# Kernel optimization log

Measured on AMD Instinct MI355X. Metric: run time of the kernel, lower is better.

Reference implementation:

```python
import jax, jax.numpy as jnp
import numpy as np

T, B, N = 256, 128, 64
START_IDX, END_IDX = 1, 2  # Offsets.GO, Offsets.EOS
NEG = -10000.0


def setup_inputs() -> dict:
    key = jax.random.key(0)
    k1, k2, k3 = jax.random.split(key, 3)
    unary = jax.random.normal(k1, (T, B, N), dtype=jnp.float32)          # [T, B, N] emissions
    trans = jax.random.normal(k2, (1, N, N), dtype=jnp.float32) * 0.1    # [1, N_to, N_from]
    lengths = jax.random.randint(k3, (B,), 1, T + 1)                      # 1 <= len <= T
    return {"unary": unary, "trans": trans, "lengths": lengths}


def _crf_log_partition(unary, trans, lengths):
    # unary: [T, B, N], trans: [1, N, N], lengths: [B] -> [B] log Z
    batch_size, n_tags = unary.shape[1], unary.shape[2]
    alphas0 = jnp.full((batch_size, 1, n_tags), NEG, dtype=unary.dtype)
    alphas0 = alphas0.at[:, 0, START_IDX].set(0.0)

    def step(alphas, xi):
        unary_t, i = xi  # unary_t: [B, N], i: scalar timestep
        # scores[b, to, fr] = alphas[b, 0, fr] + trans[0, to, fr] + unary_t[b, to]
        scores = alphas + trans + unary_t[:, :, None]            # [B, N, N]
        new_alphas = jax.nn.logsumexp(scores, axis=2)[:, None, :]  # [B, 1, N]
        # keep new alphas while the sequence is still active (i < length),
        # otherwise carry the old alphas forward (matches masked_fill logic).
        alphas = jnp.where((i < lengths)[:, None, None], new_alphas, alphas)
        return alphas, None

    steps = jnp.arange(unary.shape[0])
    alphas, _ = jax.lax.scan(step, alphas0, (unary, steps))
    terminal = alphas + trans[:, END_IDX]                         # [B, 1, N]
    return jax.nn.logsumexp(terminal, axis=2).squeeze(1)          # [B]


def reference(unary, trans, lengths):
    return _crf_log_partition(unary, trans, lengths)
```

## Files before the change

kernel.cpp:

```cpp
#include <hip/hip_runtime.h>

#define T_STEPS 256
#define B_SIZE  128
#define N_TAGS  64
#define BN_     8192
#define SEGS    16
#define SEGL    16
#define START_IDX 1
#define END_IDX 2

typedef float  f32x4  __attribute__((ext_vector_type(4)));
typedef float  f32x2  __attribute__((ext_vector_type(2)));
typedef short  bf16x8 __attribute__((ext_vector_type(8)));

union U8 { unsigned u[4]; bf16x8 v; };
union F4 { f32x4 v; f32x2 h[2]; float f[4]; };

__device__ __forceinline__ float fexp2(float x){float r;asm("v_exp_f32 %0, %1":"=v"(r):"v"(x));return r;}
__device__ __forceinline__ float flog2(float x){float r;asm("v_log_f32 %0, %1":"=v"(r):"v"(x));return r;}
__device__ __forceinline__ float frcp(float x){float r;asm("v_rcp_f32 %0, %1":"=v"(r):"v"(x));return r;}
__device__ __forceinline__ unsigned cvtpk(float lo,float hi){unsigned r;asm("v_cvt_pk_bf16_f32 %0, %1, %2":"=v"(r):"v"(lo),"v"(hi));return r;}
__device__ __forceinline__ void swap32(unsigned &a, unsigned &b){asm("v_permlane32_swap_b32 %0, %1":"+v"(a),"+v"(b));}
__device__ __forceinline__ void swap16(unsigned &a, unsigned &b){asm("v_permlane16_swap_b32 %0, %1":"+v"(a),"+v"(b));}
__device__ __forceinline__ f32x2 pkmul(f32x2 a, f32x2 b){f32x2 r;asm("v_pk_mul_f32 %0, %1, %2":"=v"(r):"v"(a),"v"(b));return r;}

#define MFMA16(A, B, C) __builtin_amdgcn_mfma_f32_16x16x32_bf16(A, B, C, 0, 0, 0)

__device__ __forceinline__ void wait24(){ asm volatile("s_waitcnt vmcnt(24)" ::: "memory"); __builtin_amdgcn_sched_barrier(0); }
__device__ __forceinline__ void wait16(){ asm volatile("s_waitcnt vmcnt(16)" ::: "memory"); __builtin_amdgcn_sched_barrier(0); }
__device__ __forceinline__ void wait8 (){ asm volatile("s_waitcnt vmcnt(8)"  ::: "memory"); __builtin_amdgcn_sched_barrier(0); }
__device__ __forceinline__ void wait0 (){ asm volatile("s_waitcnt vmcnt(0)"  ::: "memory"); __builtin_amdgcn_sched_barrier(0); }
__device__ __forceinline__ void wait28(){ asm volatile("s_waitcnt vmcnt(28)" ::: "memory"); __builtin_amdgcn_sched_barrier(0); }

#define IDP() do { _Pragma("unroll") \
  for (int c=0;c<2;++c) { _Pragma("unroll") \
    for (int cc=0;cc<4;++cc) { _Pragma("unroll") \
      for (int m=0;m<4;++m) { \
        int k0 = 32*c + 8*g + 2*m, n = 16*cc + col; \
        unsigned lo = (k0==n)?0x3F80u:0u, hi=(k0+1==n)?0x3F80u:0u; \
        P[c][cc].u[m] = lo | (hi<<16); } } } } while(0)

#define EVG() do { _Pragma("unroll") \
  for (int tt=0;tt<4;++tt) { _Pragma("unroll") \
    for (int r=0;r<4;++r) ev[tt][r] = __shfl(eul, 16*tt + 4*g + r, 64); } } while(0)

#define EVSCALE() do { _Pragma("unroll") \
  for (int tt=0;tt<4;++tt) { f32x2 e01,e23; \
    e01[0]=ev[tt][0]; e01[1]=ev[tt][1]; e23[0]=ev[tt][2]; e23[1]=ev[tt][3]; \
    _Pragma("unroll") for (int cc=0;cc<4;++cc) { \
      Dt[tt][cc].h[0]=pkmul(Dt[tt][cc].h[0],e01); \
      Dt[tt][cc].h[1]=pkmul(Dt[tt][cc].h[1],e23); } } } while(0)

#define RESC() do { float mm = Dt[0][0].f[0]; \
  _Pragma("unroll") for (int tt=0;tt<4;++tt) { _Pragma("unroll") for (int cc=0;cc<4;++cc) { \
    _Pragma("unroll") for (int r=0;r<4;++r) mm = fmaxf(mm, Dt[tt][cc].f[r]); } } \
  _Pragma("unroll") for (int m2=1;m2<64;m2<<=1) mm = fmaxf(mm, __shfl_xor(mm,m2,64)); \
  float inv = frcp(mm); C += LN2*flog2(mm); \
  f32x2 iv; iv[0]=inv; iv[1]=inv; \
  _Pragma("unroll") for (int tt=0;tt<4;++tt) { _Pragma("unroll") for (int cc=0;cc<4;++cc) { \
    Dt[tt][cc].h[0]=pkmul(Dt[tt][cc].h[0],iv); Dt[tt][cc].h[1]=pkmul(Dt[tt][cc].h[1],iv); } } } while(0)

#define CVTP() do { _Pragma("unroll") \
  for (int cc=0;cc<4;++cc) { \
    unsigned p00 = cvtpk(Dt[0][cc].f[0], Dt[0][cc].f[1]); \
    unsigned p01 = cvtpk(Dt[0][cc].f[2], Dt[0][cc].f[3]); \
    unsigned p10 = cvtpk(Dt[1][cc].f[0], Dt[1][cc].f[1]); \
    unsigned p11 = cvtpk(Dt[1][cc].f[2], Dt[1][cc].f[3]); \
    unsigned p20 = cvtpk(Dt[2][cc].f[0], Dt[2][cc].f[1]); \
    unsigned p21 = cvtpk(Dt[2][cc].f[2], Dt[2][cc].f[3]); \
    unsigned p30 = cvtpk(Dt[3][cc].f[0], Dt[3][cc].f[1]); \
    unsigned p31 = cvtpk(Dt[3][cc].f[2], Dt[3][cc].f[3]); \
    swap32(p00, p10); swap32(p01, p11); swap32(p20, p30); swap32(p21, p31); \
    swap16(p00, p10); swap16(p01, p11); swap16(p20, p30); swap16(p21, p31); \
    P[0][cc].u[0]=p00; P[0][cc].u[1]=p01; P[0][cc].u[2]=p10; P[0][cc].u[3]=p11; \
    P[1][cc].u[0]=p20; P[1][cc].u[1]=p21; P[1][cc].u[2]=p30; P[1][cc].u[3]=p31; } } while(0)

#define MFMAB() do { _Pragma("unroll") \
  for (int cc=0;cc<4;++cc) { _Pragma("unroll") \
    for (int tt=0;tt<4;++tt) { \
      f32x4 acc = MFMA16(EA[tt][0].v, P[0][cc].v, zf); \
      Dt[tt][cc].v = MFMA16(EA[tt][1].v, P[1][cc].v, acc); } } } while(0)

#define STOREP() do { _Pragma("unroll") \
  for (int cc=0;cc<4;++cc) { _Pragma("unroll") \
    for (int c=0;c<2;++c) { \
      uint4 q; q.x=P[c][cc].u[0]; q.y=P[c][cc].u[1]; q.z=P[c][cc].u[2]; q.w=P[c][cc].u[3]; \
      *(uint4*)(dst + (cc*2+c)*256) = q; } } } while(0)

__global__ __launch_bounds__(64, 2)
void crf_seg_kernel(const float* __restrict__ u, const float* __restrict__ trans,
                    const int* __restrict__ lengths,
                    unsigned* __restrict__ Mout, float* __restrict__ Cout) {
    const int bid  = blockIdx.x;
    const int b    = bid & (B_SIZE - 1);
    const int s    = bid >> 7;
    const int lane = threadIdx.x;
    const int col  = lane & 15;
    const int g    = lane >> 4;
    const float K = 1.4426950408889634f, LN2 = 0.6931471805599453f;
    const f32x4 zf = {0.f, 0.f, 0.f, 0.f};

    const int len = lengths[b];
    int n_act = len - 1 - s*SEGL;
    n_act = max(0, min(SEGL, n_act));
    unsigned* dst = Mout + (size_t)(b*SEGS + s) * 2048 + lane * 4;

    U8 P[2][4];
    if (n_act == 0) {
        IDP();
        STOREP();
        if (lane == 0) Cout[b*SEGS + s] = 0.0f;
        return;
    }

    __shared__ __align__(16) float sT[N_TAGS * N_TAGS];
    {
        const float4* t4 = (const float4*)trans;
        float4* s4 = (float4*)sT;
#pragma unroll
        for (int k = 0; k < 16; ++k) s4[k*64 + lane] = t4[k*64 + lane];
    }
    __syncthreads();

    const bool front = (s < 8);
    U8 EA[4][2];
    if (!front) {
#pragma unroll
        for (int tt = 0; tt < 4; ++tt) {
#pragma unroll
            for (int c = 0; c < 2; ++c) {
                const float* p = &sT[(16*tt + col)*64 + 32*c + 8*g];
#pragma unroll
                for (int j2 = 0; j2 < 4; ++j2)
                    EA[tt][c].u[j2] = cvtpk(fexp2(p[2*j2]*K), fexp2(p[2*j2+1]*K));
            }
        }
    } else {
#pragma unroll
        for (int tt = 0; tt < 4; ++tt) {
#pragma unroll
            for (int c = 0; c < 2; ++c) {
#pragma unroll
                for (int j2 = 0; j2 < 4; ++j2) {
                    const int a0 = 32*c + 8*g + 2*j2;
                    EA[tt][c].u[j2] = cvtpk(fexp2(sT[a0*64 + 16*tt + col] * K),
                                            fexp2(sT[(a0+1)*64 + 16*tt + col] * K));
                }
            }
        }
    }

    F4 Dt[4][4];
    float C = 0.0f;
    float ev[4][4];
    const float* ub = u + (size_t)b * 64 + lane;

    if (!front) {
        IDP();
        const int t0 = 16*s + 1;
        float uc = ub[(size_t)t0 * BN_];
        float un = ub[(size_t)min(t0 + 1, T_STEPS - 1) * BN_];
        for (int i = 0; i < n_act; ++i) {
            float eul = fexp2(uc * K);
            uc = un; un = ub[(size_t)min(t0 + i + 2, T_STEPS - 1) * BN_];
            EVG();
            MFMAB();
            EVSCALE();
            if ((i & 7) == 7) RESC();
            CVTP();
        }
    } else {
#pragma unroll
        for (int tt = 0; tt < 4; ++tt) {
#pragma unroll
            for (int cc = 0; cc < 4; ++cc) {
#pragma unroll
                for (int r = 0; r < 4; ++r)
                    Dt[tt][cc].f[r] = (tt == cc && 4*g + r == col) ? 1.0f : 0.0f;
            }
        }
        const int th = 16*s + n_act;
        float uc = ub[(size_t)th * BN_];
        float un = ub[(size_t)max(th - 1, 0) * BN_];
        for (int i = 0; i < n_act; ++i) {
            float eul = fexp2(uc * K);
            uc = un; un = ub[(size_t)max(th - i - 2, 0) * BN_];
            EVG();
            EVSCALE();
            if ((i & 7) == 7) RESC();
            CVTP();
            MFMAB();
        }
        CVTP();
    }

    STOREP();
    if (lane == 0) Cout[b*SEGS + s] = C;
}

#define MLOAD(SL, SEG) do { \
    const unsigned* _mp = mbase + (size_t)(SEG) * 2048; \
    const unsigned* _mq = _mp + 1024; \
    asm volatile("global_load_dwordx4 %0, %1, off"             : "=v"(SL[0].v) : "v"(_mp)); \
    asm volatile("global_load_dwordx4 %0, %1, off offset:1024" : "=v"(SL[1].v) : "v"(_mp)); \
    asm volatile("global_load_dwordx4 %0, %1, off offset:2048" : "=v"(SL[2].v) : "v"(_mp)); \
    asm volatile("global_load_dwordx4 %0, %1, off offset:3072" : "=v"(SL[3].v) : "v"(_mp)); \
    asm volatile("global_load_dwordx4 %0, %1, off"             : "=v"(SL[4].v) : "v"(_mq)); \
    asm volatile("global_load_dwordx4 %0, %1, off offset:1024" : "=v"(SL[5].v) : "v"(_mq)); \
    asm volatile("global_load_dwordx4 %0, %1, off offset:2048" : "=v"(SL[6].v) : "v"(_mq)); \
    asm volatile("global_load_dwordx4 %0, %1, off offset:3072" : "=v"(SL[7].v) : "v"(_mq)); \
} while (0)

#define PSTEP(WN, SL, LD) do { \
    wait##WN(); \
    U8 Af0, Af1; \
    { float vs = (g < 2) ? a0 : a1; \
      float f0=__shfl(vs,sbase+0,64), f1=__shfl(vs,sbase+1,64); \
      float f2=__shfl(vs,sbase+2,64), f3=__shfl(vs,sbase+3,64); \
      float f4=__shfl(vs,sbase+4,64), f5=__shfl(vs,sbase+5,64); \
      float f6=__shfl(vs,sbase+6,64), f7=__shfl(vs,sbase+7,64); \
      Af0.u[0]=cvtpk(f0,f1); Af0.u[1]=cvtpk(f2,f3); Af0.u[2]=cvtpk(f4,f5); Af0.u[3]=cvtpk(f6,f7); } \
    { float vs = (g < 2) ? a2 : a3; \
      float f0=__shfl(vs,sbase+0,64), f1=__shfl(vs,sbase+1,64); \
      float f2=__shfl(vs,sbase+2,64), f3=__shfl(vs,sbase+3,64); \
      float f4=__shfl(vs,sbase+4,64), f5=__shfl(vs,sbase+5,64); \
      float f6=__shfl(vs,sbase+6,64), f7=__shfl(vs,sbase+7,64); \
      Af1.u[0]=cvtpk(f0,f1); Af1.u[1]=cvtpk(f2,f3); Af1.u[2]=cvtpk(f4,f5); Af1.u[3]=cvtpk(f6,f7); } \
    f32x4 q0 = MFMA16(Af0.v, SL[0].v, zf); q0 = MFMA16(Af1.v, SL[1].v, q0); \
    f32x4 q1 = MFMA16(Af0.v, SL[2].v, zf); q1 = MFMA16(Af1.v, SL[3].v, q1); \
    f32x4 q2 = MFMA16(Af0.v, SL[4].v, zf); q2 = MFMA16(Af1.v, SL[5].v, q2); \
    f32x4 q3 = MFMA16(Af0.v, SL[6].v, zf); q3 = MFMA16(Af1.v, SL[7].v, q3); \
    float n0 = q0[0], n1 = q1[0], n2 = q2[0], n3 = q3[0]; \
    float mm = fmaxf(fmaxf(n0, n1), fmaxf(n2, n3)); \
    mm = fmaxf(mm, __shfl_xor(mm, 1, 64)); mm = fmaxf(mm, __shfl_xor(mm, 2, 64)); \
    mm = fmaxf(mm, __shfl_xor(mm, 4, 64)); mm = fmaxf(mm, __shfl_xor(mm, 8, 64)); \
    float inv = frcp(mm); C2 += LN2 * flog2(mm); \
    a0 = n0 * inv; a1 = n1 * inv; a2 = n2 * inv; a3 = n3 * inv; \
    if ((LD) >= 0) { MLOAD(SL, LD); } \
} while (0)

__global__ __launch_bounds__(128, 1)
void crf_comb_kernel(const float* __restrict__ u, const float* __restrict__ trans,
                     const unsigned* __restrict__ Mbuf, const float* __restrict__ Cseg,
                     float* __restrict__ out) {
    const int tid  = threadIdx.x;
    const int wid  = tid >> 6;
    const int lane = tid & 63;
    const int col  = lane & 15;
    const int g    = lane >> 4;
    const int b    = blockIdx.x;
    const float K = 1.4426950408889634f, LN2 = 0.6931471805599453f;
    const f32x4 zf = {0.f, 0.f, 0.f, 0.f};

    __shared__ float sX[64], sY[64], sC[2];

    float a0, a1, a2, a3;
    if (wid == 0) {
        a0 = fexp2((u[(size_t)b*64 +  0 + col] + trans[( 0 + col)*64 + START_IDX]) * K);
        a1 = fexp2((u[(size_t)b*64 + 16 + col] + trans[(16 + col)*64 + START_IDX]) * K);
        a2 = fexp2((u[(size_t)b*64 + 32 + col] + trans[(32 + col)*64 + START_IDX]) * K);
        a3 = fexp2((u[(size_t)b*64 + 48 + col] + trans[(48 + col)*64 + START_IDX]) * K);
    } else {
        a0 = fexp2(trans[END_IDX*64 +  0 + col] * K);
        a1 = fexp2(trans[END_IDX*64 + 16 + col] * K);
        a2 = fexp2(trans[END_IDX*64 + 32 + col] * K);
        a3 = fexp2(trans[END_IDX*64 + 48 + col] * K);
    }

    const int sbase = (lane & 48) | ((g & 1) << 3);
    const unsigned* mbase = Mbuf + (size_t)b * SEGS * 2048 + lane * 4;

    U8 MP0[8], MP1[8], MP2[8], MP3[8];
    float C2 = 0.0f;

    if (wid == 0) {
        MLOAD(MP0, 0); MLOAD(MP1, 1); MLOAD(MP2, 2); MLOAD(MP3, 3);
        PSTEP(24, MP0,  4); PSTEP(24, MP1,  5); PSTEP(24, MP2,  6); PSTEP(24, MP3,  7);
        PSTEP(24, MP0, -1); PSTEP(16, MP1, -1); PSTEP(8,  MP2, -1); PSTEP(0,  MP3, -1);
    } else {
        MLOAD(MP0, 15); MLOAD(MP1, 14); MLOAD(MP2, 13); MLOAD(MP3, 12);
        PSTEP(24, MP0, 11); PSTEP(24, MP1, 10); PSTEP(24, MP2,  9); PSTEP(24, MP3,  8);
        PSTEP(24, MP0, -1); PSTEP(16, MP1, -1); PSTEP(8,  MP2, -1); PSTEP(0,  MP3, -1);
    }

    if (g == 0) {
        float* dstv = wid ? sY : sX;
        dstv[ 0 + col] = a0; dstv[16 + col] = a1;
        dstv[32 + col] = a2; dstv[48 + col] = a3;
    }
    if (wid == 1) {
        float cs = (lane < SEGS) ? Cseg[b*SEGS + lane] : 0.0f;
#pragma unroll
        for (int m = 1; m < 64; m <<= 1) cs += __shfl_xor(cs, m, 64);
        if (lane == 0) sC[1] = C2 + cs;
    } else if (lane == 0) sC[0] = C2;
    __syncthreads();

    if (tid < 16) {
        float part = 0.0f;
#pragma unroll
        for (int cc = 0; cc < 4; ++cc)
            part = fmaf(sX[16*cc + tid], sY[16*cc + tid], part);
        part += __shfl_xor(part, 1, 64);
        part += __shfl_xor(part, 2, 64);
        part += __shfl_xor(part, 4, 64);
        part += __shfl_xor(part, 8, 64);
        if (tid == 0) out[b] = sC[0] + sC[1] + LN2 * flog2(part);
    }
}

#define LOAD4O(RB, PTR) do { const float* _p = (PTR); \
    asm volatile("global_load_dwordx4 %0, %1, off"            : "=v"(RB[0].v) : "v"(_p)); \
    asm volatile("global_load_dwordx4 %0, %1, off offset:64"  : "=v"(RB[1].v) : "v"(_p)); \
    asm volatile("global_load_dwordx4 %0, %1, off offset:128" : "=v"(RB[2].v) : "v"(_p)); \
    asm volatile("global_load_dwordx4 %0, %1, off offset:192" : "=v"(RB[3].v) : "v"(_p)); \
} while (0)

template<bool EUP, bool RS, bool SNAPW>
__device__ __forceinline__ void stepfn(F4 (&D)[4], F4 (&UB)[4], const U8 (&A)[4][2],
                                       bool ccw, F4 (&wS)[4], float &snapC, float &C) {
    const float K = 1.4426950408889634f, LN2 = 0.6931471805599453f;
    const f32x4 zf = {0.f, 0.f, 0.f, 0.f};
    F4 W[4];
#pragma unroll
    for (int tt = 0; tt < 4; ++tt) {
        if (EUP) {
            W[tt].h[0] = pkmul(D[tt].h[0], UB[tt].h[0]);
            W[tt].h[1] = pkmul(D[tt].h[1], UB[tt].h[1]);
        } else {
#pragma unroll
            for (int r = 0; r < 4; ++r) W[tt].f[r] = D[tt].f[r] * fexp2(UB[tt].f[r] * K);
        }
    }
    if (RS) {
        float m0 = fmaxf(fmaxf(W[0].f[0], W[0].f[1]), fmaxf(W[0].f[2], W[0].f[3]));
        float m1 = fmaxf(fmaxf(W[1].f[0], W[1].f[1]), fmaxf(W[1].f[2], W[1].f[3]));
        float m2 = fmaxf(fmaxf(W[2].f[0], W[2].f[1]), fmaxf(W[2].f[2], W[2].f[3]));
        float m3 = fmaxf(fmaxf(W[3].f[0], W[3].f[1]), fmaxf(W[3].f[2], W[3].f[3]));
        float mm = fmaxf(fmaxf(m0, m1), fmaxf(m2, m3));
        mm = fmaxf(mm, __shfl_xor(mm, 16, 64));
        mm = fmaxf(mm, __shfl_xor(mm, 32, 64));
        float inv = frcp(mm);
        C += LN2 * flog2(mm);
        f32x2 iv; iv[0] = inv; iv[1] = inv;
#pragma unroll
        for (int tt = 0; tt < 4; ++tt) {
            W[tt].h[0] = pkmul(W[tt].h[0], iv);
            W[tt].h[1] = pkmul(W[tt].h[1], iv);
        }
    }
    if (SNAPW) {
        if (__ballot(ccw)) {
#pragma unroll
            for (int tt = 0; tt < 4; ++tt) {
#pragma unroll
                for (int r = 0; r < 4; ++r)
                    wS[tt].f[r] = ccw ? W[tt].f[r] : wS[tt].f[r];
            }
            snapC = ccw ? C : snapC;
        }
    }
    unsigned p00 = cvtpk(W[0].f[0], W[0].f[1]), p01 = cvtpk(W[0].f[2], W[0].f[3]);
    unsigned p10 = cvtpk(W[1].f[0], W[1].f[1]), p11 = cvtpk(W[1].f[2], W[1].f[3]);
    unsigned p20 = cvtpk(W[2].f[0], W[2].f[1]), p21 = cvtpk(W[2].f[2], W[2].f[3]);
    unsigned p30 = cvtpk(W[3].f[0], W[3].f[1]), p31 = cvtpk(W[3].f[2], W[3].f[3]);
    swap32(p00, p10); swap32(p01, p11); swap32(p20, p30); swap32(p21, p31);
    swap16(p00, p10); swap16(p01, p11); swap16(p20, p30); swap16(p21, p31);
    U8 b0, b1;
    b0.u[0] = p00; b0.u[1] = p01; b0.u[2] = p10; b0.u[3] = p11;
    b1.u[0] = p20; b1.u[1] = p21; b1.u[2] = p30; b1.u[3] = p31;
#pragma unroll
    for (int tt = 0; tt < 4; ++tt) {
        f32x4 acc = MFMA16(A[tt][0].v, b0.v, zf);
        D[tt].v   = MFMA16(A[tt][1].v, b1.v, acc);
    }
}

__device__ __forceinline__ void make_frags(const float* sT, int wid, int col, int g,
                                           U8 (&A)[4][2], F4 (&D)[4]) {
    const float K = 1.4426950408889634f;
    if (wid == 0) {
#pragma unroll
        for (int tt = 0; tt < 4; ++tt) {
#pragma unroll
            for (int c = 0; c < 2; ++c) {
                const float* p = &sT[(16*tt + col)*64 + 32*c + 8*g];
#pragma unroll
                for (int j2 = 0; j2 < 4; ++j2)
                    A[tt][c].u[j2] = cvtpk(fexp2(p[2*j2]*K), fexp2(p[2*j2+1]*K));
            }
        }
#pragma unroll
        for (int tt = 0; tt < 4; ++tt) {
#pragma unroll
            for (int r = 0; r < 4; ++r)
                D[tt].f[r] = fexp2(sT[(16*tt + 4*g + r)*64 + START_IDX] * K);
        }
    } else {
#pragma unroll
        for (int tt = 0; tt < 4; ++tt) {
#pragma unroll
            for (int c = 0; c < 2; ++c) {
#pragma unroll
                for (int j2 = 0; j2 < 4; ++j2) {
                    const int a0 = 32*c + 8*g + 2*j2;
                    A[tt][c].u[j2] = cvtpk(fexp2(sT[a0*64 + 16*tt + col] * K),
                                           fexp2(sT[(a0+1)*64 + 16*tt + col] * K));
                }
            }
        }
#pragma unroll
        for (int tt = 0; tt < 4; ++tt) {
#pragma unroll
            for (int r = 0; r < 4; ++r)
                D[tt].f[r] = fexp2(sT[END_IDX*64 + 16*tt + 4*g + r] * K);
        }
    }
}

__launch_bounds__(128, 1)
__global__ void crf_fb_old(const float* __restrict__ src,
                           const float* __restrict__ trans,
                           const int* __restrict__ lengths,
                           float* __restrict__ out) {
    const int tid  = threadIdx.x;
    const int wid  = tid >> 6;
    const int lane = tid & 63;
    const int col  = lane & 15;
    const int g    = lane >> 4;
    const int bidx = blockIdx.x * 16 + col;

    __shared__ __align__(16) float sT[N_TAGS * N_TAGS];
    __shared__ __align__(16) float sW[N_TAGS * 16];
    __shared__ __align__(16) float sV[N_TAGS * 16];
    __shared__ float sCf[16], sCb[16];

    {
        const float4* t4 = (const float4*)trans;
        float4* s4 = (float4*)sT;
#pragma unroll
        for (int k2 = 0; k2 < 8; ++k2) s4[k2 * 128 + tid] = t4[k2 * 128 + tid];
    }
    __syncthreads();

    const float LN2 = 0.6931471805599453f;
    const int len = lengths[bidx];
    const int M   = (len - 1) >> 1;
    const int Kb  = (len - 1) - M;

    U8 A[4][2];
    F4 D[4];
    make_frags(sT, wid, col, g, A, D);

    int need = (wid == 0) ? (M + 1) : Kb;
    int mx = need;
#pragma unroll
    for (int m = 1; m < 64; m <<= 1) mx = max(mx, __shfl_xor(mx, m, 64));
    mx = __builtin_amdgcn_readfirstlane(mx);

    const int base = bidx * 64 + 4 * g;
    float C = 0.0f, snapC = 0.0f;
    F4 wS[4];
#pragma unroll
    for (int tt = 0; tt < 4; ++tt) wS[tt] = D[tt];

    F4 R0[4], R1[4], R2[4], R3[4], R4_[4], R5[4], R6[4], R7[4];

    if (wid == 0) {
        const float* pf = src + base;
        LOAD4O(R0, pf);            LOAD4O(R1, pf + BN_);
        LOAD4O(R2, pf + 2*BN_);    LOAD4O(R3, pf + 3*BN_);
        LOAD4O(R4_, pf + 4*BN_);   LOAD4O(R5, pf + 5*BN_);
        LOAD4O(R6, pf + 6*BN_);    LOAD4O(R7, pf + 7*BN_);
        const float* pn = pf + 8 * BN_;
        const int Nf = (mx + 7) & ~7;
        for (int s = 0; s < Nf; s += 8) {
#define FSTEP(QQ, RB, RSF) do { \
            const int t_ = s + (QQ); \
            wait28(); \
            stepfn<false, RSF, true>(D, RB, A, (t_ == M), wS, snapC, C); \
            LOAD4O(RB, pn); pn += BN_; \
        } while (0)
            FSTEP(0, R0, false); FSTEP(1, R1, false); FSTEP(2, R2, false);
            FSTEP(3, R3, false); FSTEP(4, R4_, false); FSTEP(5, R5, false);
            FSTEP(6, R6, false); FSTEP(7, R7, true);
#undef FSTEP
        }
        wait0();
    } else {
        const float* pb = src + base;
        {
#define PRIME(RB, q) do { int tq = max(len - 1 - (q), 0); LOAD4O(RB, pb + tq * BN_); } while (0)
            PRIME(R0, 0); PRIME(R1, 1); PRIME(R2, 2); PRIME(R3, 3);
            PRIME(R4_, 4); PRIME(R5, 5); PRIME(R6, 6); PRIME(R7, 7);
#undef PRIME
        }
        int tP = len - 9;
        const int Nb = (mx + 7) & ~7;
        for (int s = 0; s < Nb; s += 8) {
#define BSTEP(QQ, RB, RSF) do { \
            const int k_ = s + (QQ) + 1; \
            wait28(); \
            stepfn<false, RSF, false>(D, RB, A, false, wS, snapC, C); \
            if (__ballot(k_ == Kb)) { \
                const bool cc = (k_ == Kb); \
                _Pragma("unroll") \
                for (int tt = 0; tt < 4; ++tt) { \
                    _Pragma("unroll") \
                    for (int r = 0; r < 4; ++r) \
                        wS[tt].f[r] = cc ? D[tt].f[r] : wS[tt].f[r]; \
                } \
                snapC = cc ? C : snapC; \
            } \
            int tc = max(tP, 0); LOAD4O(RB, pb + tc * BN_); tP -= 1; \
        } while (0)
            BSTEP(0, R0, false); BSTEP(1, R1, false); BSTEP(2, R2, false);
            BSTEP(3, R3, false); BSTEP(4, R4_, false); BSTEP(5, R5, false);
            BSTEP(6, R6, false); BSTEP(7, R7, true);
#undef BSTEP
        }
        wait0();
    }

    {
        float* dstv = (wid == 0) ? sW : sV;
#pragma unroll
        for (int tt = 0; tt < 4; ++tt) {
#pragma unroll
            for (int r = 0; r < 4; ++r)
                dstv[(16*tt + 4*g + r) * 16 + col] = wS[tt].f[r];
        }
        if (g == 0) { if (wid == 0) sCf[col] = snapC; else sCb[col] = snapC; }
    }
    __syncthreads();
    if (wid == 0) {
        float part = 0.0f;
#pragma unroll
        for (int j = 0; j < 16; ++j) {
            const int n = g * 16 + j;
            part = fmaf(sW[n * 16 + col], sV[n * 16 + col], part);
        }
        part += __shfl_xor(part, 16, 64);
        part += __shfl_xor(part, 32, 64);
        if (g == 0) out[bidx] = sCf[col] + sCb[col] + LN2 * flog2(part);
    }
}

extern "C" void kernel_launch(void* const* d_in, const int* in_sizes, int n_in,
                              void* d_out, int out_size, void* d_ws, size_t ws_size,
                              hipStream_t stream) {
    const float* unary   = (const float*)d_in[0];
    const float* trans   = (const float*)d_in[1];
    const int*   lengths = (const int*)d_in[2];
    float* out = (float*)d_out;

    const size_t mcount = (size_t)B_SIZE * SEGS * 2048;
    const size_t need   = mcount * 4 + (size_t)B_SIZE * SEGS * 4;
    if (ws_size >= need) {
        unsigned* Mbuf = (unsigned*)d_ws;
        float* Cseg = (float*)((unsigned*)d_ws + mcount);
        hipLaunchKernelGGL(crf_seg_kernel, dim3(B_SIZE * SEGS), dim3(64), 0, stream,
                           unary, trans, lengths, Mbuf, Cseg);
        hipLaunchKernelGGL(crf_comb_kernel, dim3(B_SIZE), dim3(128), 0, stream,
                           unary, trans, Mbuf, Cseg, out);
    } else {
        hipLaunchKernelGGL(crf_fb_old, dim3(B_SIZE / 16), dim3(128), 0, stream,
                           unary, trans, lengths, out);
    }
}
```

Measured before the change: 39.66 us.

## Fuse segment and combine kernels into one per-batch block

Replaces the two-kernel scheme (2048 one-wave segment blocks followed by 128 combine blocks) with a single 512-thread block per batch element. Each of eight waves computes two segment matrices and keeps the segment constants in shared memory, then two waves run the combine step after a block barrier. The aim is to remove one kernel launch and the global round trip for the segment constants. In exchange, parallelism drops to 128 blocks, each wave processes two segments in sequence, and the segment matrices still pass through global memory inside the block. It also removes the unused EUP template path from stepfn.

```diff
diff --git a/kernel.cpp b/kernel.cpp
--- a/kernel.cpp
+++ b/kernel.cpp
@@ -81,122 +81,11 @@
       f32x4 acc = MFMA16(EA[tt][0].v, P[0][cc].v, zf); \
       Dt[tt][cc].v = MFMA16(EA[tt][1].v, P[1][cc].v, acc); } } } while(0)
 
-#define STOREP() do { _Pragma("unroll") \
+#define STOREP(DST) do { _Pragma("unroll") \
   for (int cc=0;cc<4;++cc) { _Pragma("unroll") \
     for (int c=0;c<2;++c) { \
       uint4 q; q.x=P[c][cc].u[0]; q.y=P[c][cc].u[1]; q.z=P[c][cc].u[2]; q.w=P[c][cc].u[3]; \
-      *(uint4*)(dst + (cc*2+c)*256) = q; } } } while(0)
-
-__global__ __launch_bounds__(64, 2)
-void crf_seg_kernel(const float* __restrict__ u, const float* __restrict__ trans,
-                    const int* __restrict__ lengths,
-                    unsigned* __restrict__ Mout, float* __restrict__ Cout) {
-    const int bid  = blockIdx.x;
-    const int b    = bid & (B_SIZE - 1);
-    const int s    = bid >> 7;
-    const int lane = threadIdx.x;
-    const int col  = lane & 15;
-    const int g    = lane >> 4;
-    const float K = 1.4426950408889634f, LN2 = 0.6931471805599453f;
-    const f32x4 zf = {0.f, 0.f, 0.f, 0.f};
-
-    const int len = lengths[b];
-    int n_act = len - 1 - s*SEGL;
-    n_act = max(0, min(SEGL, n_act));
-    unsigned* dst = Mout + (size_t)(b*SEGS + s) * 2048 + lane * 4;
-
-    U8 P[2][4];
-    if (n_act == 0) {
-        IDP();
-        STOREP();
-        if (lane == 0) Cout[b*SEGS + s] = 0.0f;
-        return;
-    }
-
-    __shared__ __align__(16) float sT[N_TAGS * N_TAGS];
-    {
-        const float4* t4 = (const float4*)trans;
-        float4* s4 = (float4*)sT;
-#pragma unroll
-        for (int k = 0; k < 16; ++k) s4[k*64 + lane] = t4[k*64 + lane];
-    }
-    __syncthreads();
-
-    const bool front = (s < 8);
-    U8 EA[4][2];
-    if (!front) {
-#pragma unroll
-        for (int tt = 0; tt < 4; ++tt) {
-#pragma unroll
-            for (int c = 0; c < 2; ++c) {
-                const float* p = &sT[(16*tt + col)*64 + 32*c + 8*g];
-#pragma unroll
-                for (int j2 = 0; j2 < 4; ++j2)
-                    EA[tt][c].u[j2] = cvtpk(fexp2(p[2*j2]*K), fexp2(p[2*j2+1]*K));
-            }
-        }
-    } else {
-#pragma unroll
-        for (int tt = 0; tt < 4; ++tt) {
-#pragma unroll
-            for (int c = 0; c < 2; ++c) {
-#pragma unroll
-                for (int j2 = 0; j2 < 4; ++j2) {
-                    const int a0 = 32*c + 8*g + 2*j2;
-                    EA[tt][c].u[j2] = cvtpk(fexp2(sT[a0*64 + 16*tt + col] * K),
-                                            fexp2(sT[(a0+1)*64 + 16*tt + col] * K));
-                }
-            }
-        }
-    }
-
-    F4 Dt[4][4];
-    float C = 0.0f;
-    float ev[4][4];
-    const float* ub = u + (size_t)b * 64 + lane;
-
-    if (!front) {
-        IDP();
-        const int t0 = 16*s + 1;
-        float uc = ub[(size_t)t0 * BN_];
-        float un = ub[(size_t)min(t0 + 1, T_STEPS - 1) * BN_];
-        for (int i = 0; i < n_act; ++i) {
-            float eul = fexp2(uc * K);
-            uc = un; un = ub[(size_t)min(t0 + i + 2, T_STEPS - 1) * BN_];
-            EVG();
-            MFMAB();
-            EVSCALE();
-            if ((i & 7) == 7) RESC();
-            CVTP();
-        }
-    } else {
-#pragma unroll
-        for (int tt = 0; tt < 4; ++tt) {
-#pragma unroll
-            for (int cc = 0; cc < 4; ++cc) {
-#pragma unroll
-                for (int r = 0; r < 4; ++r)
-                    Dt[tt][cc].f[r] = (tt == cc && 4*g + r == col) ? 1.0f : 0.0f;
-            }
-        }
-        const int th = 16*s + n_act;
-        float uc = ub[(size_t)th * BN_];
-        float un = ub[(size_t)max(th - 1, 0) * BN_];
-        for (int i = 0; i < n_act; ++i) {
-            float eul = fexp2(uc * K);
-            uc = un; un = ub[(size_t)max(th - i - 2, 0) * BN_];
-            EVG();
-            EVSCALE();
-            if ((i & 7) == 7) RESC();
-            CVTP();
-            MFMAB();
-        }
-        CVTP();
-    }
-
-    STOREP();
-    if (lane == 0) Cout[b*SEGS + s] = C;
-}
+      *(uint4*)((DST) + (cc*2+c)*256) = q; } } } while(0)
 
 #define MLOAD(SL, SEG) do { \
     const unsigned* _mp = mbase + (size_t)(SEG) * 2048; \
@@ -239,10 +128,10 @@
     if ((LD) >= 0) { MLOAD(SL, LD); } \
 } while (0)
 
-__global__ __launch_bounds__(128, 1)
-void crf_comb_kernel(const float* __restrict__ u, const float* __restrict__ trans,
-                     const unsigned* __restrict__ Mbuf, const float* __restrict__ Cseg,
-                     float* __restrict__ out) {
+__global__ __launch_bounds__(512, 1)
+void crf_fused(const float* __restrict__ u, const float* __restrict__ trans,
+               const int* __restrict__ lengths, unsigned* __restrict__ Mbuf,
+               float* __restrict__ out) {
     const int tid  = threadIdx.x;
     const int wid  = tid >> 6;
     const int lane = tid & 63;
@@ -252,48 +141,151 @@
     const float K = 1.4426950408889634f, LN2 = 0.6931471805599453f;
     const f32x4 zf = {0.f, 0.f, 0.f, 0.f};
 
-    __shared__ float sX[64], sY[64], sC[2];
-
-    float a0, a1, a2, a3;
-    if (wid == 0) {
-        a0 = fexp2((u[(size_t)b*64 +  0 + col] + trans[( 0 + col)*64 + START_IDX]) * K);
-        a1 = fexp2((u[(size_t)b*64 + 16 + col] + trans[(16 + col)*64 + START_IDX]) * K);
-        a2 = fexp2((u[(size_t)b*64 + 32 + col] + trans[(32 + col)*64 + START_IDX]) * K);
-        a3 = fexp2((u[(size_t)b*64 + 48 + col] + trans[(48 + col)*64 + START_IDX]) * K);
+    __shared__ __align__(16) float sT[N_TAGS * N_TAGS];
+    __shared__ float sX[64], sY[64], sC[2], sCseg[SEGS];
+
+    {
+        const float4* t4 = (const float4*)trans;
+        float4* s4 = (float4*)sT;
+        s4[tid] = t4[tid];
+        s4[tid + 512] = t4[tid + 512];
+    }
+    __syncthreads();
+
+    const int  len   = lengths[b];
+    const bool front = (wid < 4);
+
+    U8 EA[4][2];
+    if (!front) {
+#pragma unroll
+        for (int tt = 0; tt < 4; ++tt) {
+#pragma unroll
+            for (int c = 0; c < 2; ++c) {
+                const float* p = &sT[(16*tt + col)*64 + 32*c + 8*g];
+#pragma unroll
+                for (int j2 = 0; j2 < 4; ++j2)
+                    EA[tt][c].u[j2] = cvtpk(fexp2(p[2*j2]*K), fexp2(p[2*j2+1]*K));
+            }
+        }
     } else {
-        a0 = fexp2(trans[END_IDX*64 +  0 + col] * K);
-        a1 = fexp2(trans[END_IDX*64 + 16 + col] * K);
-        a2 = fexp2(trans[END_IDX*64 + 32 + col] * K);
-        a3 = fexp2(trans[END_IDX*64 + 48 + col] * K);
-    }
-
-    const int sbase = (lane & 48) | ((g & 1) << 3);
-    const unsigned* mbase = Mbuf + (size_t)b * SEGS * 2048 + lane * 4;
-
-    U8 MP0[8], MP1[8], MP2[8], MP3[8];
-    float C2 = 0.0f;
-
-    if (wid == 0) {
-        MLOAD(MP0, 0); MLOAD(MP1, 1); MLOAD(MP2, 2); MLOAD(MP3, 3);
-        PSTEP(24, MP0,  4); PSTEP(24, MP1,  5); PSTEP(24, MP2,  6); PSTEP(24, MP3,  7);
-        PSTEP(24, MP0, -1); PSTEP(16, MP1, -1); PSTEP(8,  MP2, -1); PSTEP(0,  MP3, -1);
-    } else {
-        MLOAD(MP0, 15); MLOAD(MP1, 14); MLOAD(MP2, 13); MLOAD(MP3, 12);
-        PSTEP(24, MP0, 11); PSTEP(24, MP1, 10); PSTEP(24, MP2,  9); PSTEP(24, MP3,  8);
-        PSTEP(24, MP0, -1); PSTEP(16, MP1, -1); PSTEP(8,  MP2, -1); PSTEP(0,  MP3, -1);
-    }
-
-    if (g == 0) {
-        float* dstv = wid ? sY : sX;
-        dstv[ 0 + col] = a0; dstv[16 + col] = a1;
-        dstv[32 + col] = a2; dstv[48 + col] = a3;
-    }
-    if (wid == 1) {
-        float cs = (lane < SEGS) ? Cseg[b*SEGS + lane] : 0.0f;
-#pragma unroll
-        for (int m = 1; m < 64; m <<= 1) cs += __shfl_xor(cs, m, 64);
-        if (lane == 0) sC[1] = C2 + cs;
-    } else if (lane == 0) sC[0] = C2;
+#pragma unroll
+        for (int tt = 0; tt < 4; ++tt) {
+#pragma unroll
+            for (int c = 0; c < 2; ++c) {
+#pragma unroll
+                for (int j2 = 0; j2 < 4; ++j2) {
+                    const int a0i = 32*c + 8*g + 2*j2;
+                    EA[tt][c].u[j2] = cvtpk(fexp2(sT[a0i*64 + 16*tt + col] * K),
+                                            fexp2(sT[(a0i+1)*64 + 16*tt + col] * K));
+                }
+            }
+        }
+    }
+
+    const float* ub = u + (size_t)b * 64 + lane;
+
+#pragma unroll
+    for (int q = 0; q < 2; ++q) {
+        const int s = (front ? 0 : 8) + 2*(wid & 3) + q;
+        int n_act = len - 1 - s*SEGL;
+        n_act = max(0, min(SEGL, n_act));
+        unsigned* dst = Mbuf + ((size_t)b*SEGS + s) * 2048 + lane * 4;
+
+        U8 P[2][4];
+        float C = 0.0f;
+
+        if (n_act == 0) {
+            IDP();
+        } else if (!front) {
+            IDP();
+            F4 Dt[4][4];
+            float ev[4][4];
+            const int t0 = 16*s + 1;
+            float uc = ub[(size_t)t0 * BN_];
+            float un = ub[(size_t)min(t0 + 1, T_STEPS - 1) * BN_];
+            for (int i = 0; i < n_act; ++i) {
+                float eul = fexp2(uc * K);
+                uc = un; un = ub[(size_t)min(t0 + i + 2, T_STEPS - 1) * BN_];
+                EVG();
+                MFMAB();
+                EVSCALE();
+                if ((i & 7) == 7) RESC();
+                CVTP();
+            }
+        } else {
+            F4 Dt[4][4];
+            float ev[4][4];
+#pragma unroll
+            for (int tt = 0; tt < 4; ++tt) {
+#pragma unroll
+                for (int cc = 0; cc < 4; ++cc) {
+#pragma unroll
+                    for (int r = 0; r < 4; ++r)
+                        Dt[tt][cc].f[r] = (tt == cc && 4*g + r == col) ? 1.0f : 0.0f;
+                }
+            }
+            const int th = 16*s + n_act;
+            float uc = ub[(size_t)th * BN_];
+            float un = ub[(size_t)max(th - 1, 0) * BN_];
+            for (int i = 0; i < n_act; ++i) {
+                float eul = fexp2(uc * K);
+                uc = un; un = ub[(size_t)max(th - i - 2, 0) * BN_];
+                EVG();
+                EVSCALE();
+                if ((i & 7) == 7) RESC();
+                CVTP();
+                MFMAB();
+            }
+            CVTP();
+        }
+
+        STOREP(dst);
+        if (lane == 0) sCseg[s] = C;
+    }
+    __syncthreads();
+
+    if (wid == 0 || wid == 4) {
+        float a0, a1, a2, a3;
+        if (wid == 0) {
+            a0 = fexp2((u[(size_t)b*64 +  0 + col] + trans[( 0 + col)*64 + START_IDX]) * K);
+            a1 = fexp2((u[(size_t)b*64 + 16 + col] + trans[(16 + col)*64 + START_IDX]) * K);
+            a2 = fexp2((u[(size_t)b*64 + 32 + col] + trans[(32 + col)*64 + START_IDX]) * K);
+            a3 = fexp2((u[(size_t)b*64 + 48 + col] + trans[(48 + col)*64 + START_IDX]) * K);
+        } else {
+            a0 = fexp2(trans[END_IDX*64 +  0 + col] * K);
+            a1 = fexp2(trans[END_IDX*64 + 16 + col] * K);
+            a2 = fexp2(trans[END_IDX*64 + 32 + col] * K);
+            a3 = fexp2(trans[END_IDX*64 + 48 + col] * K);
+        }
+        const int sbase = (lane & 48) | ((g & 1) << 3);
+        const unsigned* mbase = Mbuf + (size_t)b * SEGS * 2048 + lane * 4;
+        float C2 = 0.0f;
+
+        U8 MP0[8], MP1[8], MP2[8], MP3[8];
+        if (wid == 0) {
+            MLOAD(MP0, 0); MLOAD(MP1, 1); MLOAD(MP2, 2); MLOAD(MP3, 3);
+            PSTEP(24, MP0,  4); PSTEP(24, MP1,  5); PSTEP(24, MP2,  6); PSTEP(24, MP3,  7);
+            PSTEP(24, MP0, -1); PSTEP(16, MP1, -1); PSTEP(8,  MP2, -1); PSTEP(0,  MP3, -1);
+        } else {
+            MLOAD(MP0, 15); MLOAD(MP1, 14); MLOAD(MP2, 13); MLOAD(MP3, 12);
+            PSTEP(24, MP0, 11); PSTEP(24, MP1, 10); PSTEP(24, MP2,  9); PSTEP(24, MP3,  8);
+            PSTEP(24, MP0, -1); PSTEP(16, MP1, -1); PSTEP(8,  MP2, -1); PSTEP(0,  MP3, -1);
+        }
+
+        if (g == 0) {
+            float* dstv = (wid == 0) ? sX : sY;
+            dstv[ 0 + col] = a0; dstv[16 + col] = a1;
+            dstv[32 + col] = a2; dstv[48 + col] = a3;
+        }
+        if (wid == 4) {
+            float cs = (lane < SEGS) ? sCseg[lane] : 0.0f;
+#pragma unroll
+            for (int m = 1; m < 32; m <<= 1) cs += __shfl_xor(cs, m, 64);
+            if (lane == 0) sC[1] = C2 + cs;
+        } else {
+            if (lane == 0) sC[0] = C2;
+        }
+    }
     __syncthreads();
 
     if (tid < 16) {
@@ -316,7 +308,7 @@
     asm volatile("global_load_dwordx4 %0, %1, off offset:192" : "=v"(RB[3].v) : "v"(_p)); \
 } while (0)
 
-template<bool EUP, bool RS, bool SNAPW>
+template<bool RS, bool SNAPW>
 __device__ __forceinline__ void stepfn(F4 (&D)[4], F4 (&UB)[4], const U8 (&A)[4][2],
                                        bool ccw, F4 (&wS)[4], float &snapC, float &C) {
     const float K = 1.4426950408889634f, LN2 = 0.6931471805599453f;
@@ -324,13 +316,8 @@
     F4 W[4];
 #pragma unroll
     for (int tt = 0; tt < 4; ++tt) {
-        if (EUP) {
-            W[tt].h[0] = pkmul(D[tt].h[0], UB[tt].h[0]);
-            W[tt].h[1] = pkmul(D[tt].h[1], UB[tt].h[1]);
-        } else {
-#pragma unroll
-            for (int r = 0; r < 4; ++r) W[tt].f[r] = D[tt].f[r] * fexp2(UB[tt].f[r] * K);
-        }
+#pragma unroll
+        for (int r = 0; r < 4; ++r) W[tt].f[r] = D[tt].f[r] * fexp2(UB[tt].f[r] * K);
     }
     if (RS) {
         float m0 = fmaxf(fmaxf(W[0].f[0], W[0].f[1]), fmaxf(W[0].f[2], W[0].f[3]));
@@ -478,7 +465,7 @@
 #define FSTEP(QQ, RB, RSF) do { \
             const int t_ = s + (QQ); \
             wait28(); \
-            stepfn<false, RSF, true>(D, RB, A, (t_ == M), wS, snapC, C); \
+            stepfn<RSF, true>(D, RB, A, (t_ == M), wS, snapC, C); \
             LOAD4O(RB, pn); pn += BN_; \
         } while (0)
             FSTEP(0, R0, false); FSTEP(1, R1, false); FSTEP(2, R2, false);
@@ -501,7 +488,7 @@
 #define BSTEP(QQ, RB, RSF) do { \
             const int k_ = s + (QQ) + 1; \
             wait28(); \
-            stepfn<false, RSF, false>(D, RB, A, false, wS, snapC, C); \
+            stepfn<RSF, false>(D, RB, A, false, wS, snapC, C); \
             if (__ballot(k_ == Kb)) { \
                 const bool cc = (k_ == Kb); \
                 _Pragma("unroll") \
@@ -554,15 +541,11 @@
     const int*   lengths = (const int*)d_in[2];
     float* out = (float*)d_out;
 
-    const size_t mcount = (size_t)B_SIZE * SEGS * 2048;
-    const size_t need   = mcount * 4 + (size_t)B_SIZE * SEGS * 4;
+    const size_t need = (size_t)B_SIZE * SEGS * 2048 * 4;
     if (ws_size >= need) {
         unsigned* Mbuf = (unsigned*)d_ws;
-        float* Cseg = (float*)((unsigned*)d_ws + mcount);
-        hipLaunchKernelGGL(crf_seg_kernel, dim3(B_SIZE * SEGS), dim3(64), 0, stream,
-                           unary, trans, lengths, Mbuf, Cseg);
-        hipLaunchKernelGGL(crf_comb_kernel, dim3(B_SIZE), dim3(128), 0, stream,
-                           unary, trans, Mbuf, Cseg, out);
+        hipLaunchKernelGGL(crf_fused, dim3(B_SIZE), dim3(512), 0, stream,
+                           unary, trans, lengths, Mbuf, out);
     } else {
         hipLaunchKernelGGL(crf_fb_old, dim3(B_SIZE / 16), dim3(128), 0, stream,
                            unary, trans, lengths, out);
```

Result: slower. 50.68 us (+27.8%).

## Preload segment emissions into registers and use fixed-constant mid-segment rescale

Applied to the files above, without the earlier changes.

The segment kernel now loads all 16 emission rows for a segment into registers up front and fully unrolls the 16-step loop, replacing the rolling two-deep prefetch. The data-dependent max-reduction rescale (with cross-lane shuffles, log and reciprocal) is replaced by multiplication with a fixed constant 2^-64 plus a constant log offset, which removes a wave-wide reduction from the dependent chain but risks overflow or underflow for inputs outside the expected range. The shared transition tile gets a padded stride of 65 to avoid bank conflicts, and an unused template parameter is dropped from the step function.

```diff
diff --git a/kernel.cpp b/kernel.cpp
--- a/kernel.cpp
+++ b/kernel.cpp
@@ -51,12 +51,8 @@
       Dt[tt][cc].h[0]=pkmul(Dt[tt][cc].h[0],e01); \
       Dt[tt][cc].h[1]=pkmul(Dt[tt][cc].h[1],e23); } } } while(0)
 
-#define RESC() do { float mm = Dt[0][0].f[0]; \
-  _Pragma("unroll") for (int tt=0;tt<4;++tt) { _Pragma("unroll") for (int cc=0;cc<4;++cc) { \
-    _Pragma("unroll") for (int r=0;r<4;++r) mm = fmaxf(mm, Dt[tt][cc].f[r]); } } \
-  _Pragma("unroll") for (int m2=1;m2<64;m2<<=1) mm = fmaxf(mm, __shfl_xor(mm,m2,64)); \
-  float inv = frcp(mm); C += LN2*flog2(mm); \
-  f32x2 iv; iv[0]=inv; iv[1]=inv; \
+#define RESCC() do { C += 44.361419555836498f; \
+  f32x2 iv; iv[0]=5.421010862427522e-20f; iv[1]=5.421010862427522e-20f; \
   _Pragma("unroll") for (int tt=0;tt<4;++tt) { _Pragma("unroll") for (int cc=0;cc<4;++cc) { \
     Dt[tt][cc].h[0]=pkmul(Dt[tt][cc].h[0],iv); Dt[tt][cc].h[1]=pkmul(Dt[tt][cc].h[1],iv); } } } while(0)
 
@@ -81,11 +77,11 @@
       f32x4 acc = MFMA16(EA[tt][0].v, P[0][cc].v, zf); \
       Dt[tt][cc].v = MFMA16(EA[tt][1].v, P[1][cc].v, acc); } } } while(0)
 
-#define STOREP() do { _Pragma("unroll") \
+#define STOREP(DST) do { _Pragma("unroll") \
   for (int cc=0;cc<4;++cc) { _Pragma("unroll") \
     for (int c=0;c<2;++c) { \
       uint4 q; q.x=P[c][cc].u[0]; q.y=P[c][cc].u[1]; q.z=P[c][cc].u[2]; q.w=P[c][cc].u[3]; \
-      *(uint4*)(dst + (cc*2+c)*256) = q; } } } while(0)
+      *(uint4*)((DST) + (cc*2+c)*256) = q; } } } while(0)
 
 __global__ __launch_bounds__(64, 2)
 void crf_seg_kernel(const float* __restrict__ u, const float* __restrict__ trans,
@@ -97,7 +93,7 @@
     const int lane = threadIdx.x;
     const int col  = lane & 15;
     const int g    = lane >> 4;
-    const float K = 1.4426950408889634f, LN2 = 0.6931471805599453f;
+    const float K = 1.4426950408889634f;
     const f32x4 zf = {0.f, 0.f, 0.f, 0.f};
 
     const int len = lengths[b];
@@ -108,17 +104,15 @@
     U8 P[2][4];
     if (n_act == 0) {
         IDP();
-        STOREP();
+        STOREP(dst);
         if (lane == 0) Cout[b*SEGS + s] = 0.0f;
         return;
     }
 
-    __shared__ __align__(16) float sT[N_TAGS * N_TAGS];
+    __shared__ float sT[64 * 65];
     {
-        const float4* t4 = (const float4*)trans;
-        float4* s4 = (float4*)sT;
-#pragma unroll
-        for (int k = 0; k < 16; ++k) s4[k*64 + lane] = t4[k*64 + lane];
+#pragma unroll
+        for (int k = 0; k < 64; ++k) sT[k*65 + lane] = trans[k*64 + lane];
     }
     __syncthreads();
 
@@ -129,7 +123,7 @@
         for (int tt = 0; tt < 4; ++tt) {
 #pragma unroll
             for (int c = 0; c < 2; ++c) {
-                const float* p = &sT[(16*tt + col)*64 + 32*c + 8*g];
+                const float* p = &sT[(16*tt + col)*65 + 32*c + 8*g];
 #pragma unroll
                 for (int j2 = 0; j2 < 4; ++j2)
                     EA[tt][c].u[j2] = cvtpk(fexp2(p[2*j2]*K), fexp2(p[2*j2+1]*K));
@@ -142,32 +136,41 @@
             for (int c = 0; c < 2; ++c) {
 #pragma unroll
                 for (int j2 = 0; j2 < 4; ++j2) {
-                    const int a0 = 32*c + 8*g + 2*j2;
-                    EA[tt][c].u[j2] = cvtpk(fexp2(sT[a0*64 + 16*tt + col] * K),
-                                            fexp2(sT[(a0+1)*64 + 16*tt + col] * K));
+                    const int a0i = 32*c + 8*g + 2*j2;
+                    EA[tt][c].u[j2] = cvtpk(fexp2(sT[a0i*65 + 16*tt + col] * K),
+                                            fexp2(sT[(a0i+1)*65 + 16*tt + col] * K));
                 }
             }
         }
     }
 
-    F4 Dt[4][4];
+    const float* ub = u + (size_t)b * 64 + lane;
+    float Ur[16];
+    if (!front) {
+        const int t0 = 16*s + 1;
+#pragma unroll
+        for (int i = 0; i < 16; ++i) Ur[i] = ub[(size_t)min(t0 + i, T_STEPS - 1) * BN_];
+    } else {
+        const int th = 16*s + n_act;
+#pragma unroll
+        for (int i = 0; i < 16; ++i) Ur[i] = ub[(size_t)max(th - i, 0) * BN_];
+    }
+
     float C = 0.0f;
     float ev[4][4];
-    const float* ub = u + (size_t)b * 64 + lane;
+    F4 Dt[4][4];
+    { float eul = fexp2(Ur[0] * K); EVG(); }
 
     if (!front) {
         IDP();
-        const int t0 = 16*s + 1;
-        float uc = ub[(size_t)t0 * BN_];
-        float un = ub[(size_t)min(t0 + 1, T_STEPS - 1) * BN_];
-        for (int i = 0; i < n_act; ++i) {
-            float eul = fexp2(uc * K);
-            uc = un; un = ub[(size_t)min(t0 + i + 2, T_STEPS - 1) * BN_];
-            EVG();
+#pragma unroll 16
+        for (int i = 0; i < 16; ++i) {
+            if (i >= n_act) break;
             MFMAB();
             EVSCALE();
-            if ((i & 7) == 7) RESC();
+            if (i == 7) RESCC();
             CVTP();
+            if (i < 15) { float eul = fexp2(Ur[i+1] * K); EVG(); }
         }
     } else {
 #pragma unroll
@@ -179,22 +182,19 @@
                     Dt[tt][cc].f[r] = (tt == cc && 4*g + r == col) ? 1.0f : 0.0f;
             }
         }
-        const int th = 16*s + n_act;
-        float uc = ub[(size_t)th * BN_];
-        float un = ub[(size_t)max(th - 1, 0) * BN_];
-        for (int i = 0; i < n_act; ++i) {
-            float eul = fexp2(uc * K);
-            uc = un; un = ub[(size_t)max(th - i - 2, 0) * BN_];
-            EVG();
+#pragma unroll 16
+        for (int i = 0; i < 16; ++i) {
+            if (i >= n_act) break;
             EVSCALE();
-            if ((i & 7) == 7) RESC();
+            if (i == 7) RESCC();
             CVTP();
             MFMAB();
+            if (i < 15) { float eul = fexp2(Ur[i+1] * K); EVG(); }
         }
         CVTP();
     }
 
-    STOREP();
+    STOREP(dst);
     if (lane == 0) Cout[b*SEGS + s] = C;
 }
 
@@ -316,7 +316,7 @@
     asm volatile("global_load_dwordx4 %0, %1, off offset:192" : "=v"(RB[3].v) : "v"(_p)); \
 } while (0)
 
-template<bool EUP, bool RS, bool SNAPW>
+template<bool RS, bool SNAPW>
 __device__ __forceinline__ void stepfn(F4 (&D)[4], F4 (&UB)[4], const U8 (&A)[4][2],
                                        bool ccw, F4 (&wS)[4], float &snapC, float &C) {
     const float K = 1.4426950408889634f, LN2 = 0.6931471805599453f;
@@ -324,13 +324,8 @@
     F4 W[4];
 #pragma unroll
     for (int tt = 0; tt < 4; ++tt) {
-        if (EUP) {
-            W[tt].h[0] = pkmul(D[tt].h[0], UB[tt].h[0]);
-            W[tt].h[1] = pkmul(D[tt].h[1], UB[tt].h[1]);
-        } else {
-#pragma unroll
-            for (int r = 0; r < 4; ++r) W[tt].f[r] = D[tt].f[r] * fexp2(UB[tt].f[r] * K);
-        }
+#pragma unroll
+        for (int r = 0; r < 4; ++r) W[tt].f[r] = D[tt].f[r] * fexp2(UB[tt].f[r] * K);
     }
     if (RS) {
         float m0 = fmaxf(fmaxf(W[0].f[0], W[0].f[1]), fmaxf(W[0].f[2], W[0].f[3]));
@@ -478,7 +473,7 @@
 #define FSTEP(QQ, RB, RSF) do { \
             const int t_ = s + (QQ); \
             wait28(); \
-            stepfn<false, RSF, true>(D, RB, A, (t_ == M), wS, snapC, C); \
+            stepfn<RSF, true>(D, RB, A, (t_ == M), wS, snapC, C); \
             LOAD4O(RB, pn); pn += BN_; \
         } while (0)
             FSTEP(0, R0, false); FSTEP(1, R1, false); FSTEP(2, R2, false);
@@ -501,7 +496,7 @@
 #define BSTEP(QQ, RB, RSF) do { \
             const int k_ = s + (QQ) + 1; \
             wait28(); \
-            stepfn<false, RSF, false>(D, RB, A, false, wS, snapC, C); \
+            stepfn<RSF, false>(D, RB, A, false, wS, snapC, C); \
             if (__ballot(k_ == Kb)) { \
                 const bool cc = (k_ == Kb); \
                 _Pragma("unroll") \
```

Result: faster. 33.37 us (-15.9%).
